# Performance work log

Hardware: AMD Instinct MI355X
Metric: run time of the kernel (lower is better)

The kernel has to match this reference:

```python
import jax, jax.numpy as jnp
import numpy as np
from jax import lax

K = 21            # length_p_kernel
PK = K * K        # 441
CENTER = PK // 2  # 220, center of prediction window
EPS = 1e-4
PAD = K // 2


def conv3(x, w, b):
    # 3x3 same-padding conv, NCHW / OIHW
    y = lax.conv_general_dilated(x, w, (1, 1), ((1, 1), (1, 1)),
                                 dimension_numbers=('NCHW', 'OIHW', 'NCHW'))
    return y + b[None, :, None, None]


def unfold(x):
    # torch F.unfold with 21x21 kernel, zero padding 10 -> [b, C, 441, h, w]
    b, c, h, w = x.shape
    p = lax.conv_general_dilated_patches(x, (K, K), (1, 1), ((PAD, PAD), (PAD, PAD)))
    return p.reshape(b, c, PK, h, w)


def setup_inputs() -> dict:
    key = jax.random.key(0)
    ks = jax.random.split(key, 6)
    inp = jax.random.normal(ks[0], (1, 10, 128, 128), dtype=jnp.float32)
    ref = jax.random.normal(ks[1], (1, 3, 128, 128), dtype=jnp.float32)
    w0 = jax.random.normal(ks[2], (100, 10, 3, 3), dtype=jnp.float32) * 0.05
    b0 = jnp.zeros((100,), jnp.float32)
    wmid = jax.random.normal(ks[3], (23, 100, 100, 3, 3), dtype=jnp.float32) * 0.05
    bmid = jnp.zeros((23, 100), jnp.float32)
    wfin = jax.random.normal(ks[4], (441, 100, 3, 3), dtype=jnp.float32) * 0.05
    bfin = jnp.zeros((441,), jnp.float32)
    return {"input": inp, "ref": ref, "w0": w0, "b0": b0,
            "wmid": wmid, "bmid": bmid, "wfin": wfin, "bfin": bfin}


def reference(input, ref, w0, b0, wmid, bmid, wfin, bfin):
    # ref is only used by the (unavailable) loss branch; only_img_out path computed.
    b, _, h, w = input.shape

    x = conv3(input, w0, b0)

    def step(x, wb):
        return jax.nn.leaky_relu(conv3(x, wb[0], wb[1]), 0.01), None
    x, _ = lax.scan(step, x, (wmid, bmid))

    # --- W generator + softmax over 441 kernel-weight channels ---
    W = jax.nn.softmax(conv3(x, wfin, bfin), axis=1)        # [b,441,h,w]
    Wp = jnp.transpose(W, (0, 2, 3, 1))                      # [b,h,w,441]

    # --- design matrix: [1, aux features] unfolded into 21x21 windows ---
    ones = jnp.ones((b, 1, h, w), input.dtype)
    design = jnp.concatenate([ones, input[:, 3:]], axis=1)   # [b,8,h,w]
    XT = jnp.transpose(unfold(design), (0, 3, 4, 1, 2))      # [b,h,w,8,441]

    # --- weighted normal equations, per pixel ---
    XTW = XT * Wp[..., None, :]                              # [b,h,w,8,441]
    XTWX = jnp.einsum('bhwik,bhwjk->bhwij', XTW, XT)         # [b,h,w,8,8]
    reg = (jnp.eye(8, dtype=input.dtype) * EPS).at[0, 0].set(0.0)
    XTWX = XTWX + reg

    Y = jnp.transpose(unfold(input[:, :3]), (0, 3, 4, 2, 1)) # [b,h,w,441,3]
    XTWY = jnp.einsum('bhwik,bhwkc->bhwic', XTW, Y)          # [b,h,w,8,3]
    para = jnp.linalg.solve(XTWX, XTWY)                      # [b,h,w,8,3]

    # prediction at window center (loss_type == 0 path)
    domain = XT[..., CENTER]                                 # [b,h,w,8]
    out = jnp.einsum('bhwi,bhwic->bhwc', domain, para)       # [b,h,w,3]
    return jnp.transpose(out, (0, 3, 1, 2))                  # [b,3,h,w]
```

## Files before the change

kernel.cpp:

```cpp
#include <hip/hip_runtime.h>
#include <hip/hip_bf16.h>

#define HW 128
#define NPIX (HW * HW)
#define HB 130
#define HPIX (HB * HB)
#define ITW 148
#define EPS 1e-4f

typedef __attribute__((ext_vector_type(4))) float f32x4;
typedef __attribute__((ext_vector_type(2))) float f32x2;
typedef _Float16 f16;
typedef __attribute__((ext_vector_type(8))) _Float16 f16x8;
typedef __attribute__((ext_vector_type(4))) _Float16 f16x4;
typedef __attribute__((ext_vector_type(4))) int i32x4;

__device__ __forceinline__ f32x2 shflx2(f32x2 v, int m) {
  double d = __builtin_bit_cast(double, v);
  d = __shfl_xor(d, m);
  return __builtin_bit_cast(f32x2, d);
}

__global__ __launch_bounds__(256) void zero_buf(i32x4* __restrict__ p, int n) {
  int i = blockIdx.x * 256 + threadIdx.x;
  if (i < n) p[i] = i32x4{0, 0, 0, 0};
}

__global__ __launch_bounds__(256) void prep_input_k(
    const float* __restrict__ in, float* __restrict__ itp) {
  int idx = blockIdx.x * 256 + threadIdx.x;
  if (idx >= ITW * ITW) return;
  int py = idx / ITW, px = idx - py * ITW;
  float v[16];
#pragma unroll
  for (int i = 0; i < 16; i++) v[i] = 0.f;
  if (py >= 10 && py < 138 && px >= 10 && px < 138) {
    int p = (py - 10) * HW + (px - 10);
    v[0] = 1.f;
#pragma unroll
    for (int c = 0; c < 10; c++) v[1 + c] = in[c * NPIX + p];
  }
  float4* op = (float4*)(itp + idx * 16);
#pragma unroll
  for (int g = 0; g < 4; g++)
    op[g] = make_float4(v[g * 4], v[g * 4 + 1], v[g * 4 + 2], v[g * 4 + 3]);
}

__global__ __launch_bounds__(256) void pack_wmid_k(
    const float* __restrict__ wm, f16* __restrict__ wb) {
  int idx = blockIdx.x * 256 + threadIdx.x;
  int e = idx & 7;
  int l = (idx >> 3) & 63;
  int kc = (idx >> 9) & 3;
  int cf = (idx >> 11) & 7;
  int tL = idx >> 14;
  int L = tL / 9;
  int t = tL - L * 9;
  int co = cf * 16 + (l & 15);
  int ci = kc * 32 + (l >> 4) * 8 + e;
  float v = 0.f;
  if (co < 100 && ci < 100) v = wm[((L * 100 + co) * 100 + ci) * 9 + t];
  wb[idx] = (f16)v;
}

__global__ __launch_bounds__(256) void pack_wfin_k(
    const float* __restrict__ wf, f16* __restrict__ wb) {
  int idx = blockIdx.x * 256 + threadIdx.x;
  int e = idx & 7;
  int l = (idx >> 3) & 63;
  int kc = (idx >> 9) & 3;
  int cf = (idx >> 11) & 31;
  int t = idx >> 16;
  int co = cf * 16 + (l & 15);
  int ci = kc * 32 + (l >> 4) * 8 + e;
  float v = 0.f;
  if (co < 441 && ci < 100) v = wf[(co * 100 + ci) * 9 + t];
  wb[idx] = (f16)v;
}

__global__ __launch_bounds__(256) void conv0_k(
    const float* __restrict__ in, const float* __restrict__ w0,
    const float* __restrict__ b0, f16* __restrict__ act) {
  const int tx = threadIdx.x & 15, ty = threadIdx.x >> 4;
  const int x = blockIdx.x * 16 + tx, y = blockIdx.y * 16 + ty;
  const int co0 = blockIdx.z * 16;
  const int nco = max(0, min(16, 100 - co0));
  float acc[16];
#pragma unroll
  for (int i = 0; i < 16; i++) acc[i] = (i < nco) ? b0[co0 + i] : 0.f;
  for (int ci = 0; ci < 10; ci++) {
    const float* ip = in + ci * NPIX;
    float v[9];
#pragma unroll
    for (int t = 0; t < 9; t++) {
      int ny = y + t / 3 - 1, nx = x + t % 3 - 1;
      bool ok = ((unsigned)ny < (unsigned)HW) && ((unsigned)nx < (unsigned)HW);
      v[t] = ok ? ip[ny * HW + nx] : 0.f;
    }
    const float* wp = w0 + (co0 * 10 + ci) * 9;
#pragma unroll
    for (int i = 0; i < 16; i++) {
      if (i < nco) {
#pragma unroll
        for (int t = 0; t < 9; t++)
          acc[i] = fmaf(wp[i * 90 + t], v[t], acc[i]);
      }
    }
  }
  f16* op = act + ((y + 1) * HB + (x + 1)) * 128 + co0;
#pragma unroll
  for (int g = 0; g < 4; g++) {
    f16x4 sv;
#pragma unroll
    for (int j = 0; j < 4; j++) sv[j] = (f16)acc[g * 4 + j];
    *(f16x4*)(op + g * 4) = sv;
  }
}

template <int NCF, int PX, int PY, int MW, bool FINAL>
__global__ __launch_bounds__(256) void conv_mfma_k(
    const f16* __restrict__ act, const f16* __restrict__ wb,
    const float* __restrict__ bias, f16* __restrict__ out) {
  constexpr int XB = HW / PX;
  constexpr int LPW = PX + 2;
  constexpr int NN = PX / 16;
  constexpr int GEOM = (HW / PY) * XB;
  constexpr int NB = FINAL ? GEOM * 4 : GEOM;
  __shared__ f16 ldsB[(PY + 2) * LPW * 128];
  f16x8* ldsB8 = (f16x8*)ldsB;
  const f16x8* actF8 = (const f16x8*)act;
  const f16x8* wbF8 = (const f16x8*)wb;

  const int tid = threadIdx.x;
  const int l = tid & 63;
  const int w = tid >> 6;
  const int lr = l & 15;
  const int lg = l >> 4;

  const int lid = blockIdx.x;
  const int l2 = (lid & 7) * (NB >> 3) + (lid >> 3);
  const int cfq = FINAL ? (l2 / GEOM) : 0;
  const int rem = l2 % GEOM;
  const int y0 = (rem / XB) * PY;
  const int x0 = (rem % XB) * PX;
  const int cf0 = FINAL ? cfq * 8 : blockIdx.y * 4 * MW;
  const int cfw = cf0 + w * MW;

  constexpr int NCH = (PY + 2) * LPW * 16;
#pragma unroll
  for (int it = 0; it < (NCH + 255) / 256; it++) {
    int cid = it * 256 + tid;
    if (cid < NCH) {
      int row = cid / (LPW * 16);
      int rem2 = cid - row * (LPW * 16);
      int lp = rem2 >> 4;
      int c = rem2 & 15;
      f16x8 v = actF8[((y0 + row) * HB + x0 + lp) * 16 + (c ^ (lp & 7))];
      ldsB8[(row * LPW + lp) * 16 + c] = v;
    }
  }

  f16x8 af[2][MW][4];
#pragma unroll
  for (int m = 0; m < MW; m++)
#pragma unroll
    for (int kc = 0; kc < 4; kc++)
      af[0][m][kc] = wbF8[((0 * NCF + cfw + m) * 4 + kc) * 64 + l];

  __syncthreads();

  f32x4 acc[MW][NN][PY];
#pragma unroll
  for (int m = 0; m < MW; m++)
#pragma unroll
    for (int n = 0; n < NN; n++)
#pragma unroll
      for (int rr = 0; rr < PY; rr++) acc[m][n][rr] = f32x4{0.f, 0.f, 0.f, 0.f};

#pragma unroll
  for (int t = 0; t < 9; t++) {
    if (t < 8) {
#pragma unroll
      for (int m = 0; m < MW; m++)
#pragma unroll
        for (int kc = 0; kc < 4; kc++)
          af[(t + 1) & 1][m][kc] =
              wbF8[(((t + 1) * NCF + cfw + m) * 4 + kc) * 64 + l];
    }
    const int dx = t - (t / 3) * 3, r = t / 3;
    __builtin_amdgcn_s_setprio(1);
#pragma unroll
    for (int kc = 0; kc < 4; kc++) {
      const int kq = kc * 4 + lg;
      f16x8 fb[NN][PY];
#pragma unroll
      for (int n = 0; n < NN; n++)
#pragma unroll
        for (int rr = 0; rr < PY; rr++) {
          const int lp = lr + n * 16 + dx;
          fb[n][rr] = ldsB8[((r + rr) * LPW + lp) * 16 + (kq ^ (lp & 7))];
        }
#pragma unroll
      for (int m = 0; m < MW; m++)
#pragma unroll
        for (int n = 0; n < NN; n++)
#pragma unroll
          for (int rr = 0; rr < PY; rr++)
            acc[m][n][rr] = __builtin_amdgcn_mfma_f32_16x16x32_f16(
                af[t & 1][m][kc], fb[n][rr], acc[m][n][rr], 0, 0, 0);
    }
    __builtin_amdgcn_s_setprio(0);
  }

#pragma unroll
  for (int m = 0; m < MW; m++) {
#pragma unroll
    for (int n = 0; n < NN; n++) {
#pragma unroll
      for (int rr = 0; rr < PY; rr++) {
        int co = (cfw + m) * 16 + lg * 4;
        int px = x0 + n * 16 + lr;
        int yy = y0 + rr;
        if (FINAL && co >= 448) continue;
        f16x4 sv;
#pragma unroll
        for (int j = 0; j < 4; j++) {
          float v;
          if (FINAL) {
            v = (co + j < 441) ? acc[m][n][rr][j] + bias[co + j] : -60000.f;
          } else {
            float bv = (co + j < 100) ? bias[co + j] : 0.f;
            v = acc[m][n][rr][j] + bv;
            v = v > 0.f ? v : 0.01f * v;
          }
          sv[j] = (f16)v;
        }
        f16* op = FINAL ? out + (yy * HW + px) * 448 + co
                        : out + ((yy + 1) * HB + (px + 1)) * 128 + co;
        *(f16x4*)op = sv;
      }
    }
  }
}

__global__ __launch_bounds__(256) void wls_k(
    const float* __restrict__ itp, const f16* __restrict__ logits,
    float* __restrict__ out) {
  const int tid = threadIdx.x;
  const int part = tid & 15;
  const int p = blockIdx.x * 16 + (tid >> 4);
  const int x = p & (HW - 1), y = p >> 7;
  const int hpc = (y + 10) * ITW + (x + 10);

  constexpr int roff[8] = {0, 4, 8, 11, 14, 16, 18, 19};
  constexpr int rnp[8] = {4, 4, 3, 3, 2, 2, 1, 1};

  const f16* lp = logits + p * 448 + part;
  f16 lgv[28];
#pragma unroll
  for (int j = 0; j < 28; j++) lgv[j] = lp[j * 16];

  float m = -1e30f;
#pragma unroll
  for (int j = 0; j < 28; j++) m = fmaxf(m, (float)lgv[j]);
  m = fmaxf(m, __shfl_xor(m, 1));
  m = fmaxf(m, __shfl_xor(m, 2));
  m = fmaxf(m, __shfl_xor(m, 4));
  m = fmaxf(m, __shfl_xor(m, 8));

  f32x2 A2[20];
#pragma unroll
  for (int i = 0; i < 20; i++) A2[i] = f32x2{0.f, 0.f};
  f32x2 Bm2[12];
#pragma unroll
  for (int i = 0; i < 12; i++) Bm2[i] = f32x2{0.f, 0.f};
  float S = 0.f;

  int ky = 0, kx = part;
#pragma unroll
  for (int j = 0; j < 28; j++) {
    const int k = part + 16 * j;
    const float u = __expf((float)lgv[j] - m);
    S += u;
    if (k < 441) {
      const float4* q =
          (const float4*)(itp + (hpc + (ky - 10) * ITW + (kx - 10)) * 16);
      float4 f0 = q[0], f1 = q[1], f2 = q[2];
      f32x2 xv2[4] = {{f0.x, f1.x}, {f1.y, f1.z}, {f1.w, f2.x}, {f2.y, f2.z}};
      f32x2 ux2[4];
#pragma unroll
      for (int rp = 0; rp < 4; rp++) ux2[rp] = u * xv2[rp];
#pragma unroll
      for (int i = 0; i < 8; i++) {
        const float uxi = ux2[i >> 1][i & 1];
        const f32x2 sp = {uxi, uxi};
        const int b2 = (i & ~1) >> 1;
#pragma unroll
        for (int pj = 0; pj < 4; pj++) {
          if (pj < rnp[i]) A2[roff[i] + pj] = sp * xv2[b2 + pj] + A2[roff[i] + pj];
        }
      }
      const float yv[3] = {f0.y, f0.z, f0.w};
#pragma unroll
      for (int c = 0; c < 3; c++) {
        const f32x2 ys = {yv[c], yv[c]};
#pragma unroll
        for (int rp = 0; rp < 4; rp++)
          Bm2[c * 4 + rp] = ys * ux2[rp] + Bm2[c * 4 + rp];
      }
    }
    kx += 16;
    if (kx >= 21) { kx -= 21; ky += 1; }
  }

#pragma unroll
  for (int i = 0; i < 20; i++) {
    A2[i] += shflx2(A2[i], 1);
    A2[i] += shflx2(A2[i], 2);
    A2[i] += shflx2(A2[i], 4);
    A2[i] += shflx2(A2[i], 8);
  }
#pragma unroll
  for (int i = 0; i < 12; i++) {
    Bm2[i] += shflx2(Bm2[i], 1);
    Bm2[i] += shflx2(Bm2[i], 2);
    Bm2[i] += shflx2(Bm2[i], 4);
    Bm2[i] += shflx2(Bm2[i], 8);
  }
  S += __shfl_xor(S, 1);
  S += __shfl_xor(S, 2);
  S += __shfl_xor(S, 4);
  S += __shfl_xor(S, 8);

  float M[8][8], R[8][3];
#pragma unroll
  for (int i = 0; i < 8; i++) {
#pragma unroll
    for (int j = 0; j < 8; j++) {
      const int lo = (i < j) ? i : j;
      const int hi = (i < j) ? j : i;
      const int d = hi - (lo & ~1);
      M[i][j] = A2[roff[lo] + (d >> 1)][d & 1];
    }
#pragma unroll
    for (int c = 0; c < 3; c++) R[i][c] = Bm2[c * 4 + (i >> 1)][i & 1];
  }
#pragma unroll
  for (int i = 1; i < 8; i++) M[i][i] += S * EPS;

#pragma unroll
  for (int c = 0; c < 8; c++) {
    const float inv = 1.f / M[c][c];
#pragma unroll
    for (int r = c + 1; r < 8; r++) {
      const float f = M[r][c] * inv;
#pragma unroll
      for (int j = c + 1; j < 8; j++) M[r][j] = fmaf(-f, M[c][j], M[r][j]);
#pragma unroll
      for (int cc = 0; cc < 3; cc++) R[r][cc] = fmaf(-f, R[c][cc], R[r][cc]);
    }
  }
  float para[8][3];
#pragma unroll
  for (int r = 7; r >= 0; r--) {
#pragma unroll
    for (int cc = 0; cc < 3; cc++) {
      float s = R[r][cc];
#pragma unroll
      for (int j = r + 1; j < 8; j++) s = fmaf(-M[r][j], para[j][cc], s);
      para[r][cc] = s / M[r][r];
    }
  }

  const float4* qc = (const float4*)(itp + hpc * 16);
  float4 c1 = qc[1], c2 = qc[2];
  float dv[8] = {1.f, c1.x, c1.y, c1.z, c1.w, c2.x, c2.y, c2.z};
  if (part < 3) {
    float res = 0.f;
#pragma unroll
    for (int i = 0; i < 8; i++) res = fmaf(dv[i], para[i][part], res);
    out[part * NPIX + p] = res;
  }
}

extern "C" void kernel_launch(void* const* d_in, const int* in_sizes, int n_in,
                              void* d_out, int out_size, void* d_ws, size_t ws_size,
                              hipStream_t stream) {
  const float* input = (const float*)d_in[0];
  const float* w0 = (const float*)d_in[2];
  const float* b0 = (const float*)d_in[3];
  const float* wmid = (const float*)d_in[4];
  const float* bmid = (const float*)d_in[5];
  const float* wfin = (const float*)d_in[6];
  const float* bfin = (const float*)d_in[7];
  float* out = (float*)d_out;

  f16* act0 = (f16*)d_ws;
  f16* act1 = act0 + HPIX * 128;
  f16* logits = act1 + HPIX * 128;
  f16* wbuf = logits + NPIX * 448;
  f16* wfbuf = wbuf + 23 * 9 * 16384;
  float* inputT = (float*)(wfbuf + 9 * 65536);

  {
    int n = (2 * HPIX * 128 * 2) / 16;
    zero_buf<<<(n + 255) / 256, 256, 0, stream>>>((i32x4*)act0, n);
  }
  prep_input_k<<<(ITW * ITW + 255) / 256, 256, 0, stream>>>(input, inputT);
  pack_wmid_k<<<(23 * 9 * 16384) / 256, 256, 0, stream>>>(wmid, wbuf);
  pack_wfin_k<<<(9 * 65536) / 256, 256, 0, stream>>>(wfin, wfbuf);

  conv0_k<<<dim3(8, 8, 8), 256, 0, stream>>>(input, w0, b0, act0);

  for (int L = 0; L < 23; L++) {
    const f16* src = (L & 1) ? act1 : act0;
    f16* dst = (L & 1) ? act0 : act1;
    conv_mfma_k<8, 16, 4, 1, false><<<dim3(256, 2), 256, 0, stream>>>(
        src, wbuf + (long)L * 9 * 16384, bmid + L * 100, dst);
  }
  conv_mfma_k<32, 32, 4, 2, true><<<dim3(512), 256, 0, stream>>>(
      act1, wfbuf, bfin, logits);

  wls_k<<<NPIX * 16 / 256, 256, 0, stream>>>(inputT, logits, out);
}
```

Measured before the change: 327.9 us.

## Switch convolutions to 32x32x16 MFMA tiles and widen WLS reduction to 32 lanes

The convolution kernel moves from 16x16x32 to 32x32x16 f16 MFMA. The weight packing layout is rewritten for 32-channel output groups and 16-channel K chunks. Tiles become 32 pixels wide with a smaller row count, so the mid layers run as one 512-block launch and the final conv as 1024 blocks. The WLS kernel now splits each pixel across 32 lanes instead of 16, which adds a shuffle reduction step but gives more threads per pixel. Together these aim to raise MFMA throughput and occupancy, at the cost of less weight reuse per block and extra reduction work.

```diff
diff --git a/kernel.cpp b/kernel.cpp
--- a/kernel.cpp
+++ b/kernel.cpp
@@ -8,6 +8,7 @@
 #define ITW 148
 #define EPS 1e-4f
 
+typedef __attribute__((ext_vector_type(16))) float f32x16;
 typedef __attribute__((ext_vector_type(4))) float f32x4;
 typedef __attribute__((ext_vector_type(2))) float f32x2;
 typedef _Float16 f16;
@@ -51,13 +52,13 @@
   int idx = blockIdx.x * 256 + threadIdx.x;
   int e = idx & 7;
   int l = (idx >> 3) & 63;
-  int kc = (idx >> 9) & 3;
-  int cf = (idx >> 11) & 7;
+  int kc = (idx >> 9) & 7;
+  int cg = (idx >> 12) & 3;
   int tL = idx >> 14;
   int L = tL / 9;
   int t = tL - L * 9;
-  int co = cf * 16 + (l & 15);
-  int ci = kc * 32 + (l >> 4) * 8 + e;
+  int co = cg * 32 + (l & 31);
+  int ci = kc * 16 + (l >> 5) * 8 + e;
   float v = 0.f;
   if (co < 100 && ci < 100) v = wm[((L * 100 + co) * 100 + ci) * 9 + t];
   wb[idx] = (f16)v;
@@ -68,11 +69,11 @@
   int idx = blockIdx.x * 256 + threadIdx.x;
   int e = idx & 7;
   int l = (idx >> 3) & 63;
-  int kc = (idx >> 9) & 3;
-  int cf = (idx >> 11) & 31;
+  int kc = (idx >> 9) & 7;
+  int cg = (idx >> 12) & 15;
   int t = idx >> 16;
-  int co = cf * 16 + (l & 15);
-  int ci = kc * 32 + (l >> 4) * 8 + e;
+  int co = cg * 32 + (l & 31);
+  int ci = kc * 16 + (l >> 5) * 8 + e;
   float v = 0.f;
   if (co < 441 && ci < 100) v = wf[(co * 100 + ci) * 9 + t];
   wb[idx] = (f16)v;
@@ -117,13 +118,13 @@
   }
 }
 
-template <int NCF, int PX, int PY, int MW, bool FINAL>
+template <int NCG, int PY, bool FINAL>
 __global__ __launch_bounds__(256) void conv_mfma_k(
     const f16* __restrict__ act, const f16* __restrict__ wb,
     const float* __restrict__ bias, f16* __restrict__ out) {
+  constexpr int PX = 32;
   constexpr int XB = HW / PX;
   constexpr int LPW = PX + 2;
-  constexpr int NN = PX / 16;
   constexpr int GEOM = (HW / PY) * XB;
   constexpr int NB = FINAL ? GEOM * 4 : GEOM;
   __shared__ f16 ldsB[(PY + 2) * LPW * 128];
@@ -134,8 +135,8 @@
   const int tid = threadIdx.x;
   const int l = tid & 63;
   const int w = tid >> 6;
-  const int lr = l & 15;
-  const int lg = l >> 4;
+  const int lc = l & 31;
+  const int lh = l >> 5;
 
   const int lid = blockIdx.x;
   const int l2 = (lid & 7) * (NB >> 3) + (lid >> 3);
@@ -143,8 +144,7 @@
   const int rem = l2 % GEOM;
   const int y0 = (rem / XB) * PY;
   const int x0 = (rem % XB) * PX;
-  const int cf0 = FINAL ? cfq * 8 : blockIdx.y * 4 * MW;
-  const int cfw = cf0 + w * MW;
+  const int cgw = (FINAL ? cfq * 4 : 0) + w;
 
   constexpr int NCH = (PY + 2) * LPW * 16;
 #pragma unroll
@@ -160,85 +160,68 @@
     }
   }
 
-  f16x8 af[2][MW][4];
-#pragma unroll
-  for (int m = 0; m < MW; m++)
-#pragma unroll
-    for (int kc = 0; kc < 4; kc++)
-      af[0][m][kc] = wbF8[((0 * NCF + cfw + m) * 4 + kc) * 64 + l];
+  f16x8 af[2][8];
+#pragma unroll
+  for (int kc = 0; kc < 8; kc++)
+    af[0][kc] = wbF8[((0 * NCG + cgw) * 8 + kc) * 64 + l];
 
   __syncthreads();
 
-  f32x4 acc[MW][NN][PY];
-#pragma unroll
-  for (int m = 0; m < MW; m++)
-#pragma unroll
-    for (int n = 0; n < NN; n++)
-#pragma unroll
-      for (int rr = 0; rr < PY; rr++) acc[m][n][rr] = f32x4{0.f, 0.f, 0.f, 0.f};
+  f32x16 acc[PY];
+#pragma unroll
+  for (int rr = 0; rr < PY; rr++)
+#pragma unroll
+    for (int j = 0; j < 16; j++) acc[rr][j] = 0.f;
 
 #pragma unroll
   for (int t = 0; t < 9; t++) {
     if (t < 8) {
 #pragma unroll
-      for (int m = 0; m < MW; m++)
-#pragma unroll
-        for (int kc = 0; kc < 4; kc++)
-          af[(t + 1) & 1][m][kc] =
-              wbF8[(((t + 1) * NCF + cfw + m) * 4 + kc) * 64 + l];
+      for (int kc = 0; kc < 8; kc++)
+        af[(t + 1) & 1][kc] = wbF8[(((t + 1) * NCG + cgw) * 8 + kc) * 64 + l];
     }
     const int dx = t - (t / 3) * 3, r = t / 3;
+    const int lp = lc + dx;
     __builtin_amdgcn_s_setprio(1);
 #pragma unroll
-    for (int kc = 0; kc < 4; kc++) {
-      const int kq = kc * 4 + lg;
-      f16x8 fb[NN][PY];
-#pragma unroll
-      for (int n = 0; n < NN; n++)
-#pragma unroll
-        for (int rr = 0; rr < PY; rr++) {
-          const int lp = lr + n * 16 + dx;
-          fb[n][rr] = ldsB8[((r + rr) * LPW + lp) * 16 + (kq ^ (lp & 7))];
+    for (int kc = 0; kc < 8; kc++) {
+      const int c = kc * 2 + lh;
+      f16x8 fb[PY];
+#pragma unroll
+      for (int rr = 0; rr < PY; rr++)
+        fb[rr] = ldsB8[((r + rr) * LPW + lp) * 16 + (c ^ (lp & 7))];
+#pragma unroll
+      for (int rr = 0; rr < PY; rr++)
+        acc[rr] = __builtin_amdgcn_mfma_f32_32x32x16_f16(
+            af[t & 1][kc], fb[rr], acc[rr], 0, 0, 0);
+    }
+    __builtin_amdgcn_s_setprio(0);
+  }
+
+#pragma unroll
+  for (int rr = 0; rr < PY; rr++) {
+    const int px = x0 + lc;
+    const int yy = y0 + rr;
+#pragma unroll
+    for (int q = 0; q < 4; q++) {
+      int co = cgw * 32 + 8 * q + 4 * lh;
+      if (FINAL && co >= 448) continue;
+      f16x4 sv;
+#pragma unroll
+      for (int j = 0; j < 4; j++) {
+        float v;
+        if (FINAL) {
+          v = (co + j < 441) ? acc[rr][q * 4 + j] + bias[co + j] : -60000.f;
+        } else {
+          float bv = (co + j < 100) ? bias[co + j] : 0.f;
+          v = acc[rr][q * 4 + j] + bv;
+          v = v > 0.f ? v : 0.01f * v;
         }
-#pragma unroll
-      for (int m = 0; m < MW; m++)
-#pragma unroll
-        for (int n = 0; n < NN; n++)
-#pragma unroll
-          for (int rr = 0; rr < PY; rr++)
-            acc[m][n][rr] = __builtin_amdgcn_mfma_f32_16x16x32_f16(
-                af[t & 1][m][kc], fb[n][rr], acc[m][n][rr], 0, 0, 0);
-    }
-    __builtin_amdgcn_s_setprio(0);
-  }
-
-#pragma unroll
-  for (int m = 0; m < MW; m++) {
-#pragma unroll
-    for (int n = 0; n < NN; n++) {
-#pragma unroll
-      for (int rr = 0; rr < PY; rr++) {
-        int co = (cfw + m) * 16 + lg * 4;
-        int px = x0 + n * 16 + lr;
-        int yy = y0 + rr;
-        if (FINAL && co >= 448) continue;
-        f16x4 sv;
-#pragma unroll
-        for (int j = 0; j < 4; j++) {
-          float v;
-          if (FINAL) {
-            v = (co + j < 441) ? acc[m][n][rr][j] + bias[co + j] : -60000.f;
-          } else {
-            float bv = (co + j < 100) ? bias[co + j] : 0.f;
-            v = acc[m][n][rr][j] + bv;
-            v = v > 0.f ? v : 0.01f * v;
-          }
-          sv[j] = (f16)v;
-        }
-        f16* op = FINAL ? out + (yy * HW + px) * 448 + co
-                        : out + ((yy + 1) * HB + (px + 1)) * 128 + co;
-        *(f16x4*)op = sv;
+        sv[j] = (f16)v;
       }
+      f16* op = FINAL ? out + (yy * HW + px) * 448 + co
+                      : out + ((yy + 1) * HB + (px + 1)) * 128 + co;
+      *(f16x4*)op = sv;
     }
   }
 }
@@ -247,8 +230,8 @@
     const float* __restrict__ itp, const f16* __restrict__ logits,
     float* __restrict__ out) {
   const int tid = threadIdx.x;
-  const int part = tid & 15;
-  const int p = blockIdx.x * 16 + (tid >> 4);
+  const int part = tid & 31;
+  const int p = blockIdx.x * 8 + (tid >> 5);
   const int x = p & (HW - 1), y = p >> 7;
   const int hpc = (y + 10) * ITW + (x + 10);
 
@@ -256,17 +239,18 @@
   constexpr int rnp[8] = {4, 4, 3, 3, 2, 2, 1, 1};
 
   const f16* lp = logits + p * 448 + part;
-  f16 lgv[28];
-#pragma unroll
-  for (int j = 0; j < 28; j++) lgv[j] = lp[j * 16];
+  f16 lgv[14];
+#pragma unroll
+  for (int j = 0; j < 14; j++) lgv[j] = lp[j * 32];
 
   float m = -1e30f;
 #pragma unroll
-  for (int j = 0; j < 28; j++) m = fmaxf(m, (float)lgv[j]);
+  for (int j = 0; j < 14; j++) m = fmaxf(m, (float)lgv[j]);
   m = fmaxf(m, __shfl_xor(m, 1));
   m = fmaxf(m, __shfl_xor(m, 2));
   m = fmaxf(m, __shfl_xor(m, 4));
   m = fmaxf(m, __shfl_xor(m, 8));
+  m = fmaxf(m, __shfl_xor(m, 16));
 
   f32x2 A2[20];
 #pragma unroll
@@ -276,13 +260,14 @@
   for (int i = 0; i < 12; i++) Bm2[i] = f32x2{0.f, 0.f};
   float S = 0.f;
 
-  int ky = 0, kx = part;
-#pragma unroll
-  for (int j = 0; j < 28; j++) {
-    const int k = part + 16 * j;
+#pragma unroll
+  for (int j = 0; j < 14; j++) {
+    const int k = part + 32 * j;
     const float u = __expf((float)lgv[j] - m);
     S += u;
     if (k < 441) {
+      const int ky = k / 21;
+      const int kx = k - ky * 21;
       const float4* q =
           (const float4*)(itp + (hpc + (ky - 10) * ITW + (kx - 10)) * 16);
       float4 f0 = q[0], f1 = q[1], f2 = q[2];
@@ -309,8 +294,6 @@
           Bm2[c * 4 + rp] = ys * ux2[rp] + Bm2[c * 4 + rp];
       }
     }
-    kx += 16;
-    if (kx >= 21) { kx -= 21; ky += 1; }
   }
 
 #pragma unroll
@@ -319,6 +302,7 @@
     A2[i] += shflx2(A2[i], 2);
     A2[i] += shflx2(A2[i], 4);
     A2[i] += shflx2(A2[i], 8);
+    A2[i] += shflx2(A2[i], 16);
   }
 #pragma unroll
   for (int i = 0; i < 12; i++) {
@@ -326,11 +310,13 @@
     Bm2[i] += shflx2(Bm2[i], 2);
     Bm2[i] += shflx2(Bm2[i], 4);
     Bm2[i] += shflx2(Bm2[i], 8);
+    Bm2[i] += shflx2(Bm2[i], 16);
   }
   S += __shfl_xor(S, 1);
   S += __shfl_xor(S, 2);
   S += __shfl_xor(S, 4);
   S += __shfl_xor(S, 8);
+  S += __shfl_xor(S, 16);
 
   float M[8][8], R[8][3];
 #pragma unroll
@@ -415,11 +401,11 @@
   for (int L = 0; L < 23; L++) {
     const f16* src = (L & 1) ? act1 : act0;
     f16* dst = (L & 1) ? act0 : act1;
-    conv_mfma_k<8, 16, 4, 1, false><<<dim3(256, 2), 256, 0, stream>>>(
+    conv_mfma_k<4, 1, false><<<dim3(512), 256, 0, stream>>>(
         src, wbuf + (long)L * 9 * 16384, bmid + L * 100, dst);
   }
-  conv_mfma_k<32, 32, 4, 2, true><<<dim3(512), 256, 0, stream>>>(
+  conv_mfma_k<16, 2, true><<<dim3(1024), 256, 0, stream>>>(
       act1, wfbuf, bfin, logits);
 
-  wls_k<<<NPIX * 16 / 256, 256, 0, stream>>>(inputT, logits, out);
-}
+  wls_k<<<NPIX / 8, 256, 0, stream>>>(inputT, logits, out);
+}
```

Measured after the change: 364.7 us. 11.2% more time.

## Split K across two wave groups in mid convs with LDS reduction

Applied to the files above, without the earlier changes.

Replaces the templated mid-layer conv with a dedicated 512-thread kernel. Each of the four output-channel waves is duplicated, and each copy handles half of the input-channel reduction. The partial sums are then combined through shared memory before bias and leaky ReLU are applied. The aim is more waves per block to hide latency in these small 23 layers, at the cost of an extra LDS round trip and a second barrier. The final conv becomes a non-templated-FINAL specialization with the same behaviour.

```diff
diff --git a/kernel.cpp b/kernel.cpp
--- a/kernel.cpp
+++ b/kernel.cpp
@@ -117,15 +117,116 @@
   }
 }
 
-template <int NCF, int PX, int PY, int MW, bool FINAL>
-__global__ __launch_bounds__(256) void conv_mfma_k(
+__global__ __launch_bounds__(512) void conv_mid_k(
+    const f16* __restrict__ act, const f16* __restrict__ wb,
+    const float* __restrict__ bias, f16* __restrict__ out) {
+  constexpr int PX = 16, PY = 4, LPW = PX + 2, XB = HW / PX;
+  constexpr int NB = (HW / PY) * XB;
+  __shared__ f16 ldsB[(PY + 2) * LPW * 128];
+  __shared__ f32x4 ldsR[4][64][PY];
+  f16x8* ldsB8 = (f16x8*)ldsB;
+  const f16x8* actF8 = (const f16x8*)act;
+  const f16x8* wbF8 = (const f16x8*)wb;
+
+  const int tid = threadIdx.x;
+  const int l = tid & 63;
+  const int w = tid >> 6;
+  const int q = w & 3;
+  const int kh = w >> 2;
+  const int lr = l & 15;
+  const int lg = l >> 4;
+
+  const int lid = blockIdx.x;
+  const int l2 = (lid & 7) * (NB >> 3) + (lid >> 3);
+  const int y0 = (l2 / XB) * PY;
+  const int x0 = (l2 % XB) * PX;
+  const int cfw = blockIdx.y * 4 + q;
+
+  constexpr int NCH = (PY + 2) * LPW * 16;
+#pragma unroll
+  for (int it = 0; it < (NCH + 511) / 512; it++) {
+    int cid = it * 512 + tid;
+    if (cid < NCH) {
+      int row = cid / (LPW * 16);
+      int rem2 = cid - row * (LPW * 16);
+      int lp = rem2 >> 4;
+      int c = rem2 & 15;
+      f16x8 v = actF8[((y0 + row) * HB + x0 + lp) * 16 + (c ^ (lp & 7))];
+      ldsB8[(row * LPW + lp) * 16 + c] = v;
+    }
+  }
+
+  f16x8 af[2][2];
+#pragma unroll
+  for (int kc2 = 0; kc2 < 2; kc2++)
+    af[0][kc2] = wbF8[((0 * 8 + cfw) * 4 + kh * 2 + kc2) * 64 + l];
+
+  __syncthreads();
+
+  f32x4 acc[PY];
+#pragma unroll
+  for (int rr = 0; rr < PY; rr++) acc[rr] = f32x4{0.f, 0.f, 0.f, 0.f};
+
+#pragma unroll
+  for (int t = 0; t < 9; t++) {
+    if (t < 8) {
+#pragma unroll
+      for (int kc2 = 0; kc2 < 2; kc2++)
+        af[(t + 1) & 1][kc2] =
+            wbF8[(((t + 1) * 8 + cfw) * 4 + kh * 2 + kc2) * 64 + l];
+    }
+    const int dx = t - (t / 3) * 3, r = t / 3;
+    const int lp = lr + dx;
+    __builtin_amdgcn_s_setprio(1);
+#pragma unroll
+    for (int kc2 = 0; kc2 < 2; kc2++) {
+      const int kq = (kh * 2 + kc2) * 4 + lg;
+      f16x8 fb[PY];
+#pragma unroll
+      for (int rr = 0; rr < PY; rr++)
+        fb[rr] = ldsB8[((r + rr) * LPW + lp) * 16 + (kq ^ (lp & 7))];
+#pragma unroll
+      for (int rr = 0; rr < PY; rr++)
+        acc[rr] = __builtin_amdgcn_mfma_f32_16x16x32_f16(
+            af[t & 1][kc2], fb[rr], acc[rr], 0, 0, 0);
+    }
+    __builtin_amdgcn_s_setprio(0);
+  }
+
+  if (kh == 1) {
+#pragma unroll
+    for (int rr = 0; rr < PY; rr++) ldsR[q][l][rr] = acc[rr];
+  }
+  __syncthreads();
+  if (kh == 0) {
+#pragma unroll
+    for (int rr = 0; rr < PY; rr++) {
+      f32x4 o = ldsR[q][l][rr];
+      const int co = cfw * 16 + lg * 4;
+      const int px = x0 + lr;
+      const int yy = y0 + rr;
+      f16x4 sv;
+#pragma unroll
+      for (int j = 0; j < 4; j++) {
+        float bv = (co + j < 100) ? bias[co + j] : 0.f;
+        float v = acc[rr][j] + o[j] + bv;
+        v = v > 0.f ? v : 0.01f * v;
+        sv[j] = (f16)v;
+      }
+      *(f16x4*)(out + ((yy + 1) * HB + (px + 1)) * 128 + co) = sv;
+    }
+  }
+}
+
+template <int NCF, int PX, int PY, int MW>
+__global__ __launch_bounds__(256) void conv_fin_k(
     const f16* __restrict__ act, const f16* __restrict__ wb,
     const float* __restrict__ bias, f16* __restrict__ out) {
   constexpr int XB = HW / PX;
   constexpr int LPW = PX + 2;
   constexpr int NN = PX / 16;
   constexpr int GEOM = (HW / PY) * XB;
-  constexpr int NB = FINAL ? GEOM * 4 : GEOM;
+  constexpr int NB = GEOM * 4;
   __shared__ f16 ldsB[(PY + 2) * LPW * 128];
   f16x8* ldsB8 = (f16x8*)ldsB;
   const f16x8* actF8 = (const f16x8*)act;
@@ -139,11 +240,11 @@
 
   const int lid = blockIdx.x;
   const int l2 = (lid & 7) * (NB >> 3) + (lid >> 3);
-  const int cfq = FINAL ? (l2 / GEOM) : 0;
+  const int cfq = l2 / GEOM;
   const int rem = l2 % GEOM;
   const int y0 = (rem / XB) * PY;
   const int x0 = (rem % XB) * PX;
-  const int cf0 = FINAL ? cfq * 8 : blockIdx.y * 4 * MW;
+  const int cf0 = cfq * 8;
   const int cfw = cf0 + w * MW;
 
   constexpr int NCH = (PY + 2) * LPW * 16;
@@ -221,23 +322,14 @@
         int co = (cfw + m) * 16 + lg * 4;
         int px = x0 + n * 16 + lr;
         int yy = y0 + rr;
-        if (FINAL && co >= 448) continue;
+        if (co >= 448) continue;
         f16x4 sv;
 #pragma unroll
         for (int j = 0; j < 4; j++) {
-          float v;
-          if (FINAL) {
-            v = (co + j < 441) ? acc[m][n][rr][j] + bias[co + j] : -60000.f;
-          } else {
-            float bv = (co + j < 100) ? bias[co + j] : 0.f;
-            v = acc[m][n][rr][j] + bv;
-            v = v > 0.f ? v : 0.01f * v;
-          }
+          float v = (co + j < 441) ? acc[m][n][rr][j] + bias[co + j] : -60000.f;
           sv[j] = (f16)v;
         }
-        f16* op = FINAL ? out + (yy * HW + px) * 448 + co
-                        : out + ((yy + 1) * HB + (px + 1)) * 128 + co;
-        *(f16x4*)op = sv;
+        *(f16x4*)(out + (yy * HW + px) * 448 + co) = sv;
       }
     }
   }
@@ -415,10 +507,10 @@
   for (int L = 0; L < 23; L++) {
     const f16* src = (L & 1) ? act1 : act0;
     f16* dst = (L & 1) ? act0 : act1;
-    conv_mfma_k<8, 16, 4, 1, false><<<dim3(256, 2), 256, 0, stream>>>(
+    conv_mid_k<<<dim3(256, 2), 512, 0, stream>>>(
         src, wbuf + (long)L * 9 * 16384, bmid + L * 100, dst);
   }
-  conv_mfma_k<32, 32, 4, 2, true><<<dim3(512), 256, 0, stream>>>(
+  conv_fin_k<32, 32, 4, 2><<<dim3(512), 256, 0, stream>>>(
       act1, wfbuf, bfin, logits);
 
   wls_k<<<NPIX * 16 / 256, 256, 0, stream>>>(inputT, logits, out);
```

After: 328.0 us. No clear change (+0.1%).
